# Optimization experiments

Measured on AMD Instinct MI355X. Metric: run time of the kernel, lower is better.

## Reference

```python
import jax, jax.numpy as jnp
import numpy as np
import math

B, S, H = 2, 2048, 2048
NH, HD = 16, 64  # head_dim = H // (2*NH)
LAMBDA_INIT = 0.5


def setup_inputs() -> dict:
    key = jax.random.key(0)
    ks = jax.random.split(key, 6)
    std = 1.0 / math.sqrt(H)
    hidden_states = jax.random.normal(ks[0], (B, S, H), dtype=jnp.float32)
    # Linear weights stored as [in, out] (x @ W)
    Wq = jax.random.normal(ks[1], (H, 2 * NH * HD), dtype=jnp.float32) * std
    Wk = jax.random.normal(ks[2], (H, 2 * NH * HD), dtype=jnp.float32) * std
    Wv = jax.random.normal(ks[3], (H, NH * HD), dtype=jnp.float32) * std
    Wo = jax.random.normal(ks[4], (NH * HD, H), dtype=jnp.float32) * (1.0 / math.sqrt(NH * HD))
    lambda_param = jnp.log(jnp.asarray(1.0 / math.tanh(LAMBDA_INIT), dtype=jnp.float32))
    # causal additive mask, (B, 1, S, S)
    causal = jnp.tril(jnp.ones((S, S), dtype=bool))
    attention_mask = jnp.where(causal, 0.0, jnp.finfo(jnp.float32).min)[None, None]
    attention_mask = jnp.broadcast_to(attention_mask, (B, 1, S, S))
    return {"hidden_states": hidden_states, "attention_mask": attention_mask,
            "Wq": Wq, "Wk": Wk, "Wv": Wv, "Wo": Wo, "lambda_param": lambda_param}


def reference(hidden_states, attention_mask, Wq, Wk, Wv, Wo, lambda_param):
    bsz, q_len, _ = hidden_states.shape
    scaling = HD ** -0.5

    q_all = (hidden_states @ Wq).reshape(bsz, q_len, 2 * NH, HD).transpose(0, 2, 1, 3)
    k_all = (hidden_states @ Wk).reshape(bsz, q_len, 2 * NH, HD).transpose(0, 2, 1, 3)
    v = (hidden_states @ Wv).reshape(bsz, q_len, NH, HD).transpose(0, 2, 1, 3)
    q1, q2 = q_all[:, :NH], q_all[:, NH:]
    k1, k2 = k_all[:, :NH], k_all[:, NH:]

    lam = jnp.tanh(jax.nn.softplus(lambda_param))
    scores1 = jnp.einsum('bhqd,bhkd->bhqk', q1, k1) * scaling
    scores2 = jnp.einsum('bhqd,bhkd->bhqk', q2, k2) * scaling
    attn_scores = scores1 - lam * scores2 + attention_mask
    attn_weights = jax.nn.softmax(attn_scores.astype(jnp.float32), axis=-1).astype(q1.dtype)

    attn_out = jnp.einsum('bhqk,bhkd->bhqd', attn_weights, v)
    attn_out = attn_out.transpose(0, 2, 1, 3).reshape(bsz, q_len, NH * HD)
    return attn_out @ Wo
```

## Files before the change

kernel.cpp:

```cpp
#include <hip/hip_runtime.h>
#include <hip/hip_bf16.h>

#define B_ 2
#define S_ 2048
#define H_ 2048
#define NH_ 16
#define HD_ 64
#define DQ_ 2048
#define DV_ 1024
#define QKS_ 4096

using bf16x8 = __attribute__((ext_vector_type(8))) __bf16;
using f32x4  = __attribute__((ext_vector_type(4))) float;

typedef __attribute__((address_space(1))) unsigned int u32g;
typedef __attribute__((address_space(3))) unsigned int u32l;

__device__ __forceinline__ void gload_lds16(const __bf16* g, __bf16* l) {
  __builtin_amdgcn_global_load_lds((u32g*)g, (u32l*)l, 16, 0, 0);
}

__device__ __forceinline__ int swz(int row, int colb, int strideB) {
  return row * strideB + (colb ^ (((row ^ (row >> 3)) & 7) << 4));
}
__device__ __forceinline__ int fxor(int row) { return (row ^ (row >> 3)) & 7; }


__global__ __launch_bounds__(256) void cast_hidden(const float* __restrict__ in,
                                                   __bf16* __restrict__ out, int n) {
  int i = (blockIdx.x * 256 + threadIdx.x) * 8;
  if (i >= n) return;
  float4 a = *reinterpret_cast<const float4*>(in + i);
  float4 b = *reinterpret_cast<const float4*>(in + i + 4);
  bf16x8 o;
  o[0] = (__bf16)a.x; o[1] = (__bf16)a.y; o[2] = (__bf16)a.z; o[3] = (__bf16)a.w;
  o[4] = (__bf16)b.x; o[5] = (__bf16)b.y; o[6] = (__bf16)b.z; o[7] = (__bf16)b.w;
  *reinterpret_cast<bf16x8*>(out + i) = o;
}

__global__ __launch_bounds__(256) void transpose_cast(const float* __restrict__ in,
                                                      __bf16* __restrict__ out, int R, int C) {
  __shared__ float tile[32][33];
  int tx = threadIdx.x & 31, ty = threadIdx.x >> 5;
  int c0 = blockIdx.x * 32, r0 = blockIdx.y * 32;
  for (int i = 0; i < 32; i += 8)
    tile[ty + i][tx] = in[(size_t)(r0 + ty + i) * C + c0 + tx];
  __syncthreads();
  for (int i = 0; i < 32; i += 8)
    out[(size_t)(c0 + ty + i) * R + r0 + tx] = (__bf16)tile[tx][ty + i];
}


template <typename OutT>
__global__ __launch_bounds__(256) void gemm_bt(const __bf16* __restrict__ A,
                                               const __bf16* __restrict__ Bt,
                                               OutT* __restrict__ C,
                                               int M, int N, int K) {
  __shared__ __bf16 As[2][128 * 32];
  __shared__ __bf16 Bs[2][128 * 32];
  const int nx = gridDim.x;
  int id = blockIdx.y * nx + blockIdx.x;
  const int cpx = (nx * gridDim.y) >> 3;
  id = (id & 7) * cpx + (id >> 3);
  const int bm = id / nx, bn = id % nx;

  const int tid = threadIdx.x;
  const int wid = tid >> 6, lane = tid & 63;
  const int wm = wid >> 1, wn = wid & 1;
  const int g = lane >> 4, c = lane & 15;

  f32x4 acc[4][4] = {};
  const __bf16* Abase = A + (size_t)(bm * 128) * K;
  const __bf16* Bbase = Bt + (size_t)(bn * 128) * K;
  const int srow = wid * 16 + (lane >> 2);
  const int scol = (lane & 3) * 8;
  const int nk = K >> 5;

  auto stage = [&](int p, int kt) {
    int k0 = kt * 32;
    gload_lds16(Abase + (size_t)srow * K + k0 + scol,        &As[p][(wid * 16) * 32]);
    gload_lds16(Abase + (size_t)(srow + 64) * K + k0 + scol, &As[p][(64 + wid * 16) * 32]);
    gload_lds16(Bbase + (size_t)srow * K + k0 + scol,        &Bs[p][(wid * 16) * 32]);
    gload_lds16(Bbase + (size_t)(srow + 64) * K + k0 + scol, &Bs[p][(64 + wid * 16) * 32]);
  };

  stage(0, 0);
  stage(1, 1);

  for (int kt = 0; kt < nk; ++kt) {
    const int p = kt & 1;
    if (kt + 1 < nk) {
      asm volatile("s_waitcnt vmcnt(4)" ::: "memory");
    } else {
      asm volatile("s_waitcnt vmcnt(0)" ::: "memory");
    }
    __builtin_amdgcn_s_barrier();
    __builtin_amdgcn_sched_barrier(0);

    bf16x8 af[4], bfv[4];
#pragma unroll
    for (int i = 0; i < 4; ++i)
      af[i] = *reinterpret_cast<const bf16x8*>(&As[p][(wm * 64 + i * 16 + c) * 32 + g * 8]);
#pragma unroll
    for (int i = 0; i < 4; ++i)
      bfv[i] = *reinterpret_cast<const bf16x8*>(&Bs[p][(wn * 64 + i * 16 + c) * 32 + g * 8]);
#pragma unroll
    for (int m = 0; m < 4; ++m)
#pragma unroll
      for (int n = 0; n < 4; ++n)
        acc[m][n] = __builtin_amdgcn_mfma_f32_16x16x32_bf16(af[m], bfv[n], acc[m][n], 0, 0, 0);

    __builtin_amdgcn_sched_barrier(0);
    __builtin_amdgcn_s_barrier();
    if (kt + 2 < nk) stage(p, kt + 2);
  }

#pragma unroll
  for (int m = 0; m < 4; ++m)
#pragma unroll
    for (int n = 0; n < 4; ++n)
#pragma unroll
      for (int r = 0; r < 4; ++r) {
        int row = bm * 128 + wm * 64 + m * 16 + g * 4 + r;
        int col = bn * 128 + wn * 64 + n * 16 + c;
        float v = acc[m][n][r];
        if constexpr (sizeof(OutT) == 2)
          C[(size_t)row * N + col] = (OutT)(__bf16)v;
        else
          C[(size_t)row * N + col] = v;
      }
}


template <typename OutT>
__global__ __launch_bounds__(512, 2) void gemm256(const __bf16* __restrict__ A,
                                                  const __bf16* __restrict__ Bt,
                                                  OutT* __restrict__ C,
                                                  int M, int N, int K) {
  __shared__ __bf16 As[2][256 * 64];
  __shared__ __bf16 Bs[2][256 * 64];
  const int nx = gridDim.x;
  int id = blockIdx.y * nx + blockIdx.x;
  const int cpx = (nx * gridDim.y) >> 3;
  id = (id & 7) * cpx + (id >> 3);
  const int bm = id / nx, bn = id % nx;

  const int tid = threadIdx.x;
  const int wid = tid >> 6, lane = tid & 63;
  const int wm = wid >> 2, wn = wid & 3;
  const int g = lane >> 4, c = lane & 15;

  f32x4 acc[8][4] = {};
  bf16x8 af[4][2];
  bf16x8 bfv[4][2];
  const __bf16* Abase = A + (size_t)(bm * 256) * K;
  const __bf16* Bbase = Bt + (size_t)(bn * 256) * K;
  const int niter = K >> 7;

  auto stageA = [&](int p, int half, int kt) {
#pragma unroll
    for (int j = 0; j < 2; ++j) {
      int row = half * 128 + j * 64 + wid * 8 + (lane >> 3);
      int gc = (lane & 7) ^ (row & 7);
      gload_lds16(Abase + (size_t)row * K + kt * 64 + gc * 8,
                  &As[p][(half * 128 + j * 64 + wid * 8) * 64]);
    }
  };
  auto stageB = [&](int p, int half, int kt) {
#pragma unroll
    for (int j = 0; j < 2; ++j) {
      int row = half * 128 + j * 64 + wid * 8 + (lane >> 3);
      int gc = (lane & 7) ^ (row & 7);
      gload_lds16(Bbase + (size_t)row * K + kt * 64 + gc * 8,
                  &Bs[p][(half * 128 + j * 64 + wid * 8) * 64]);
    }
  };
  auto readA = [&](int p, int m, int kk) -> bf16x8 {
    int row = wm * 128 + m * 16 + c;
    int ch = (kk * 4 + g) ^ (row & 7);
    return *reinterpret_cast<const bf16x8*>(&As[p][row * 64 + ch * 8]);
  };
  auto readB = [&](int p, int n, int kk) -> bf16x8 {
    int row = wn * 64 + n * 16 + c;
    int ch = (kk * 4 + g) ^ (row & 7);
    return *reinterpret_cast<const bf16x8*>(&Bs[p][row * 64 + ch * 8]);
  };
  auto quad = [&](int mb, int nb) {
    __builtin_amdgcn_s_setprio(1);
#pragma unroll
    for (int mi = 0; mi < 4; ++mi)
#pragma unroll
      for (int ni = 0; ni < 2; ++ni)
#pragma unroll
        for (int kk = 0; kk < 2; ++kk)
          acc[mb + mi][nb + ni] = __builtin_amdgcn_mfma_f32_16x16x32_bf16(
              af[mi][kk], bfv[nb + ni][kk], acc[mb + mi][nb + ni], 0, 0, 0);
    __builtin_amdgcn_s_setprio(0);
  };
#define BAR1_LGKM()  __builtin_amdgcn_s_barrier(); \
    asm volatile("s_waitcnt lgkmcnt(0)" ::: "memory"); \
    __builtin_amdgcn_sched_barrier(0)
#define BAR2()  __builtin_amdgcn_sched_barrier(0); __builtin_amdgcn_s_barrier()

  stageA(0, 0, 0); stageA(0, 1, 0);
  stageB(0, 0, 0); stageB(0, 1, 0);
  stageB(1, 0, 1); stageB(1, 1, 1);
  asm volatile("s_waitcnt vmcnt(0)" ::: "memory");
  __builtin_amdgcn_s_barrier();

  for (int i = 0; i < niter; ++i) {
    const int t1 = 2 * i + 1;
    const bool more = (i + 1 < niter);
#pragma unroll
    for (int mi = 0; mi < 4; ++mi) { af[mi][0] = readA(0, mi, 0); af[mi][1] = readA(0, mi, 1); }
#pragma unroll
    for (int ni = 0; ni < 2; ++ni) { bfv[ni][0] = readB(0, ni, 0); bfv[ni][1] = readB(0, ni, 1); }
    stageA(1, 0, t1);
    BAR1_LGKM(); quad(0, 0); BAR2();
#pragma unroll
    for (int ni = 2; ni < 4; ++ni) { bfv[ni][0] = readB(0, ni, 0); bfv[ni][1] = readB(0, ni, 1); }
    stageA(1, 1, t1);
    BAR1_LGKM(); quad(0, 2); BAR2();
#pragma unroll
    for (int mi = 0; mi < 4; ++mi) { af[mi][0] = readA(0, 4 + mi, 0); af[mi][1] = readA(0, 4 + mi, 1); }
    if (more) stageB(0, 0, t1 + 1);
    BAR1_LGKM(); quad(4, 0); BAR2();
    if (more) {
      stageB(0, 1, t1 + 1);
      asm volatile("s_waitcnt vmcnt(4)" ::: "memory");
    } else {
      asm volatile("s_waitcnt vmcnt(0)" ::: "memory");
    }
    __builtin_amdgcn_s_barrier();
    __builtin_amdgcn_sched_barrier(0);
    quad(4, 2); BAR2();
#pragma unroll
    for (int mi = 0; mi < 4; ++mi) { af[mi][0] = readA(1, mi, 0); af[mi][1] = readA(1, mi, 1); }
#pragma unroll
    for (int ni = 0; ni < 2; ++ni) { bfv[ni][0] = readB(1, ni, 0); bfv[ni][1] = readB(1, ni, 1); }
    if (more) stageA(0, 0, t1 + 1);
    BAR1_LGKM(); quad(0, 0); BAR2();
#pragma unroll
    for (int ni = 2; ni < 4; ++ni) { bfv[ni][0] = readB(1, ni, 0); bfv[ni][1] = readB(1, ni, 1); }
    if (more) stageA(0, 1, t1 + 1);
    BAR1_LGKM(); quad(0, 2); BAR2();
#pragma unroll
    for (int mi = 0; mi < 4; ++mi) { af[mi][0] = readA(1, 4 + mi, 0); af[mi][1] = readA(1, 4 + mi, 1); }
    if (more) stageB(1, 0, t1 + 2);
    BAR1_LGKM(); quad(4, 0); BAR2();
    if (more) {
      stageB(1, 1, t1 + 2);
      asm volatile("s_waitcnt vmcnt(4)" ::: "memory");
    } else {
      asm volatile("s_waitcnt vmcnt(0)" ::: "memory");
    }
    __builtin_amdgcn_s_barrier();
    __builtin_amdgcn_sched_barrier(0);
    quad(4, 2); BAR2();
  }
#undef BAR1_LGKM
#undef BAR2

#pragma unroll
  for (int m = 0; m < 8; ++m)
#pragma unroll
    for (int n = 0; n < 4; ++n)
#pragma unroll
      for (int r = 0; r < 4; ++r) {
        int row = bm * 256 + wm * 128 + m * 16 + g * 4 + r;
        int col = bn * 256 + wn * 64 + n * 16 + c;
        float v = acc[m][n][r];
        if constexpr (sizeof(OutT) == 2)
          C[(size_t)row * N + col] = (OutT)(__bf16)v;
        else
          C[(size_t)row * N + col] = v;
      }
}


__global__ __launch_bounds__(256, 2) void diffattn(const __bf16* __restrict__ QK,
                                                   const __bf16* __restrict__ V,
                                                   __bf16* __restrict__ OpA,
                                                   __bf16* __restrict__ OpB,
                                                   float* __restrict__ ml,
                                                   const float* __restrict__ lambda_param) {
  __shared__ __bf16 Ks[2][64 * 128];
  __shared__ __bf16 Vs[2][64 * 64];
  __shared__ __bf16 Ps[128 * 64];

  const int y = blockIdx.y;
  const int qt = ((y >> 4) & 1) ? blockIdx.x : (gridDim.x - 1 - blockIdx.x);
  const int bh = y >> 1;
  const int half = y & 1;
  const int b = bh >> 4, h = bh & 15;
  const int tid = threadIdx.x;
  const int w = tid >> 6, lane = tid & 63;
  const int g = lane >> 4, c = lane & 15;
  const float NEG_INF = -__builtin_inff();

  const float lam = tanhf(log1pf(__expf(lambda_param[0])));
  const float L2E = 1.4426950408889634f;
  const float sc1 = 0.125f * L2E;
  const float sc2 = -lam * 0.125f * L2E;

  bf16x8 qf[2][4];
#pragma unroll
  for (int fr = 0; fr < 2; ++fr) {
    int qrow = qt * 128 + w * 32 + fr * 16 + c;
    const __bf16* qbase = QK + (size_t)(b * S_ + qrow) * QKS_;
#pragma unroll
    for (int kk = 0; kk < 4; ++kk) {
      int d = kk * 32 + g * 8;
      const __bf16* src = (d < 64) ? (qbase + h * 64 + d)
                                   : (qbase + DV_ + h * 64 + (d - 64));
      float s = (d < 64) ? sc1 : sc2;
      bf16x8 raw = *reinterpret_cast<const bf16x8*>(src);
      bf16x8 ov;
#pragma unroll
      for (int i = 0; i < 8; ++i) ov[i] = (__bf16)((float)raw[i] * s);
      qf[fr][kk] = ov;
    }
  }

  f32x4 acc[2][4] = {};
  float mrow[2][4], lrow[2][4];
#pragma unroll
  for (int fr = 0; fr < 2; ++fr)
#pragma unroll
    for (int r = 0; r < 4; ++r) { mrow[fr][r] = -1e30f; lrow[fr][r] = 0.f; }

  const int kt0 = half ? (qt + 1) : 0;
  const int kt1 = half ? (2 * qt + 2) : (qt + 1);

  auto stageK = [&](int p, int kt) {
#pragma unroll
    for (int j = 0; j < 4; ++j) {
      int row = w * 16 + j * 4 + (lane >> 4);
      int gc = (lane & 15) ^ fxor(row);
      int s = kt * 64 + row;
      const __bf16* kbase = QK + (size_t)(b * S_ + s) * QKS_ + 2048;
      const __bf16* src = (gc < 8) ? (kbase + h * 64 + gc * 8)
                                   : (kbase + DV_ + h * 64 + (gc - 8) * 8);
      gload_lds16(src, &Ks[p][(w * 16 + j * 4) * 128]);
    }
  };
  auto loadV = [&](int kt, bf16x8* vv) {
#pragma unroll
    for (int j = 0; j < 2; ++j) {
      int flat = tid + j * 256;
      int kv = flat >> 3;
      int d = (flat & 7) * 8;
      vv[j] = *reinterpret_cast<const bf16x8*>(
          V + (size_t)(b * S_ + kt * 64 + kv) * DV_ + h * 64 + d);
    }
  };
  auto scatterV = [&](int p, const bf16x8* vv) {
    char* VsB = (char*)Vs[p];
#pragma unroll
    for (int j = 0; j < 2; ++j) {
      int flat = tid + j * 256;
      int kv = flat >> 3;
      int d = (flat & 7) * 8;
#pragma unroll
      for (int i = 0; i < 8; ++i)
        *reinterpret_cast<__bf16*>(VsB + swz(d + i, kv * 2, 128)) = vv[j][i];
    }
  };

  {
    stageK(0, kt0);
    bf16x8 vv[2];
    loadV(kt0, vv);
    scatterV(0, vv);
    __syncthreads();
  }

  for (int kt = kt0; kt < kt1; ++kt) {
    const int p = (kt - kt0) & 1;
    const bool pre = (kt + 1 < kt1);
    bf16x8 vv[2];
    if (pre) {
      stageK(p ^ 1, kt + 1);
      loadV(kt + 1, vv);
    }

    f32x4 sc[2][4] = {};
    char* KsB = (char*)Ks[p];
    __builtin_amdgcn_s_setprio(1);
#pragma unroll
    for (int f = 0; f < 4; ++f)
#pragma unroll
      for (int kk = 0; kk < 4; ++kk) {
        bf16x8 kf = *reinterpret_cast<const bf16x8*>(
            KsB + swz(f * 16 + c, (kk * 32 + g * 8) * 2, 256));
        sc[0][f] = __builtin_amdgcn_mfma_f32_16x16x32_bf16(qf[0][kk], kf, sc[0][f], 0, 0, 0);
        sc[1][f] = __builtin_amdgcn_mfma_f32_16x16x32_bf16(qf[1][kk], kf, sc[1][f], 0, 0, 0);
      }
    __builtin_amdgcn_s_setprio(0);

    const int dz = kt - 2 * qt;
#pragma unroll
    for (int fr = 0; fr < 2; ++fr) {
      const int wrow0 = w * 32 + fr * 16;
      float pmax[4] = {NEG_INF, NEG_INF, NEG_INF, NEG_INF};
      if (dz >= 0) {
#pragma unroll
        for (int f = 0; f < 4; ++f)
#pragma unroll
          for (int r = 0; r < 4; ++r) {
            float s = sc[fr][f][r];
            if (dz * 64 + f * 16 + c > wrow0 + g * 4 + r) s = NEG_INF;
            sc[fr][f][r] = s;
            pmax[r] = fmaxf(pmax[r], s);
          }
      } else {
#pragma unroll
        for (int f = 0; f < 4; ++f)
#pragma unroll
          for (int r = 0; r < 4; ++r)
            pmax[r] = fmaxf(pmax[r], sc[fr][f][r]);
      }

      float dm = NEG_INF;
#pragma unroll
      for (int r = 0; r < 4; ++r) dm = fmaxf(dm, pmax[r] - mrow[fr][r]);
      if (!__all(dm <= 8.0f)) {
#pragma unroll
        for (int m = 1; m < 16; m <<= 1)
#pragma unroll
          for (int r = 0; r < 4; ++r)
            pmax[r] = fmaxf(pmax[r], __shfl_xor(pmax[r], m, 64));
        float pscl[4];
#pragma unroll
        for (int r = 0; r < 4; ++r) {
          float mnew = fmaxf(mrow[fr][r], pmax[r]);
          pscl[r] = __builtin_amdgcn_exp2f(mrow[fr][r] - mnew);
          mrow[fr][r] = mnew;
        }
#pragma unroll
        for (int r = 0; r < 4; ++r) lrow[fr][r] *= pscl[r];
#pragma unroll
        for (int n = 0; n < 4; ++n)
#pragma unroll
          for (int r = 0; r < 4; ++r)
            acc[fr][n][r] *= pscl[r];
      }

      float rowsum[4] = {0.f, 0.f, 0.f, 0.f};
#pragma unroll
      for (int f = 0; f < 4; ++f)
#pragma unroll
        for (int r = 0; r < 4; ++r) {
          float pv = __builtin_amdgcn_exp2f(sc[fr][f][r] - mrow[fr][r]);
          sc[fr][f][r] = pv;
          rowsum[r] += pv;
        }
#pragma unroll
      for (int m = 1; m < 16; m <<= 1)
#pragma unroll
        for (int r = 0; r < 4; ++r)
          rowsum[r] += __shfl_xor(rowsum[r], m, 64);
#pragma unroll
      for (int r = 0; r < 4; ++r)
        lrow[fr][r] += rowsum[r];

      char* PsB = (char*)Ps;
#pragma unroll
      for (int f = 0; f < 4; ++f)
#pragma unroll
        for (int r = 0; r < 4; ++r)
          *reinterpret_cast<__bf16*>(
              PsB + swz(wrow0 + g * 4 + r, (f * 16 + c) * 2, 128)) = (__bf16)sc[fr][f][r];
    }

    {
      char* PsB = (char*)Ps;
      char* VsB = (char*)Vs[p];
      __builtin_amdgcn_s_setprio(1);
#pragma unroll
      for (int fr = 0; fr < 2; ++fr)
#pragma unroll
        for (int kc = 0; kc < 2; ++kc) {
          bf16x8 pf = *reinterpret_cast<const bf16x8*>(
              PsB + swz(w * 32 + fr * 16 + c, (kc * 32 + g * 8) * 2, 128));
#pragma unroll
          for (int n = 0; n < 4; ++n) {
            bf16x8 vf = *reinterpret_cast<const bf16x8*>(
                VsB + swz(n * 16 + c, (kc * 32 + g * 8) * 2, 128));
            acc[fr][n] = __builtin_amdgcn_mfma_f32_16x16x32_bf16(pf, vf, acc[fr][n], 0, 0, 0);
          }
        }
      __builtin_amdgcn_s_setprio(0);
    }

    if (pre) scatterV(p ^ 1, vv);
    __syncthreads();
  }

  __bf16* Op = half ? OpB : OpA;
#pragma unroll
  for (int fr = 0; fr < 2; ++fr)
#pragma unroll
    for (int n = 0; n < 4; ++n)
#pragma unroll
      for (int r = 0; r < 4; ++r) {
        int q = qt * 128 + w * 32 + fr * 16 + g * 4 + r;
        Op[(size_t)(b * S_ + q) * DV_ + h * 64 + n * 16 + c] = (__bf16)acc[fr][n][r];
      }
  if (c == 0) {
#pragma unroll
    for (int fr = 0; fr < 2; ++fr)
#pragma unroll
      for (int r = 0; r < 4; ++r) {
        int q = qt * 128 + w * 32 + fr * 16 + g * 4 + r;
        float2 v;
        v.x = mrow[fr][r];
        v.y = lrow[fr][r];
        *reinterpret_cast<float2*>(&ml[((size_t)(half * 32 + bh) * S_ + q) * 2]) = v;
      }
  }
}


__global__ __launch_bounds__(256) void merge_halves(const __bf16* __restrict__ OpA,
                                                    const __bf16* __restrict__ OpB,
                                                    const float* __restrict__ ml,
                                                    __bf16* __restrict__ AO) {
  int flat = blockIdx.x * 256 + threadIdx.x;
  int d0 = (flat & 7) * 8;
  int row = flat >> 3;
  int bh = row >> 11, q = row & 2047;
  int b = bh >> 4, h = bh & 15;
  size_t obase = (size_t)(b * S_ + q) * DV_ + h * 64 + d0;

  float2 a2 = *reinterpret_cast<const float2*>(&ml[((size_t)bh * S_ + q) * 2]);
  float2 b2 = *reinterpret_cast<const float2*>(&ml[((size_t)(32 + bh) * S_ + q) * 2]);
  float m = fmaxf(a2.x, b2.x);
  float wA = __builtin_amdgcn_exp2f(a2.x - m);
  float wB = __builtin_amdgcn_exp2f(b2.x - m);
  float inv = 1.0f / (a2.y * wA + b2.y * wB);
  wA *= inv; wB *= inv;

  bf16x8 oa = *reinterpret_cast<const bf16x8*>(OpA + obase);
  bf16x8 ob = *reinterpret_cast<const bf16x8*>(OpB + obase);
  bf16x8 o;
#pragma unroll
  for (int i = 0; i < 8; ++i)
    o[i] = (__bf16)((float)oa[i] * wA + (float)ob[i] * wB);
  *reinterpret_cast<bf16x8*>(AO + obase) = o;
}


extern "C" void kernel_launch(void* const* d_in, const int* in_sizes, int n_in,
                              void* d_out, int out_size, void* d_ws, size_t ws_size,
                              hipStream_t stream) {
  const float* hidden = (const float*)d_in[0];
  const float* Wq = (const float*)d_in[2];
  const float* Wk = (const float*)d_in[3];
  const float* Wv = (const float*)d_in[4];
  const float* Wo = (const float*)d_in[5];
  const float* lambda_param = (const float*)d_in[6];
  float* out = (float*)d_out;

  char* ws = (char*)d_ws;
  size_t off = 0;
  auto alloc = [&](size_t bytes) {
    void* p = ws + off;
    off += (bytes + 255) & ~(size_t)255;
    return p;
  };
  const int M = B_ * S_;
  __bf16* hidb = (__bf16*)alloc((size_t)M * H_ * 2);
  __bf16* TB   = (__bf16*)alloc((size_t)QKS_ * H_ * 2);
  __bf16* QKa  = (__bf16*)alloc((size_t)M * QKS_ * 2);
  __bf16* Va   = (__bf16*)((char*)TB + 4u * 1024 * 1024);
  float*  mlb  = (float*)((char*)TB + 12u * 1024 * 1024);
  __bf16* OpA  = hidb;
  __bf16* OpB  = hidb + (size_t)M * DV_;
  __bf16* AO   = hidb;
  (void)ws_size; (void)in_sizes; (void)n_in; (void)out_size;

  int nh = M * H_;
  cast_hidden<<<nh / (256 * 8), 256, 0, stream>>>(hidden, hidb, nh);

  transpose_cast<<<dim3(DQ_ / 32, H_ / 32), 256, 0, stream>>>(Wq, TB, H_, DQ_);
  transpose_cast<<<dim3(DQ_ / 32, H_ / 32), 256, 0, stream>>>(Wk, TB + (size_t)DQ_ * H_, H_, DQ_);
  gemm256<__bf16><<<dim3(QKS_ / 256, M / 256), 512, 0, stream>>>(hidb, TB, QKa, M, QKS_, H_);

  transpose_cast<<<dim3(DV_ / 32, H_ / 32), 256, 0, stream>>>(Wv, TB, H_, DV_);
  gemm_bt<__bf16><<<dim3(DV_ / 128, M / 128), 256, 0, stream>>>(hidb, TB, Va, M, DV_, H_);

  diffattn<<<dim3(S_ / 128, B_ * NH_ * 2), 256, 0, stream>>>(QKa, Va, OpA, OpB, mlb, lambda_param);
  merge_halves<<<(B_ * NH_ * S_ * HD_ / 8) / 256, 256, 0, stream>>>(OpA, OpB, mlb, AO);

  transpose_cast<<<dim3(H_ / 32, DV_ / 32), 256, 0, stream>>>(Wo, TB, DV_, H_);
  gemm_bt<float><<<dim3(H_ / 128, M / 128), 256, 0, stream>>>(AO, TB, out, M, H_, DV_);
}
```

Before: 250.9 us.

## Compute transposed S^T tiles and feed P to PV MFMA via shuffles

The QK^T MFMA operands are swapped so each lane owns a full query row's scores. Row max and sum then need only two cross-lane shuffles instead of four per row, and the softmax probabilities are packed into bf16 and redistributed with lane shuffles straight into the PV MFMA operand, removing the Ps shared-memory round trip. The output accumulators come out transposed, so the partial outputs are stored d-major and merge_halves now transposes through shared memory. This adds many shuffles per tile and a strided output layout in exchange for less LDS traffic and fewer reductions.

```diff
diff --git a/kernel.cpp b/kernel.cpp
--- a/kernel.cpp
+++ b/kernel.cpp
@@ -24,6 +24,14 @@
   return row * strideB + (colb ^ (((row ^ (row >> 3)) & 7) << 4));
 }
 __device__ __forceinline__ int fxor(int row) { return (row ^ (row >> 3)) & 7; }
+
+__device__ __forceinline__ unsigned int pk2(float a, float b) {
+  __bf16 ba = (__bf16)a, bb = (__bf16)b;
+  unsigned short ua, ub;
+  __builtin_memcpy(&ua, &ba, 2);
+  __builtin_memcpy(&ub, &bb, 2);
+  return (unsigned int)ua | ((unsigned int)ub << 16);
+}
 
 
 __global__ __launch_bounds__(256) void cast_hidden(const float* __restrict__ in,
@@ -286,7 +294,6 @@
                                                    const float* __restrict__ lambda_param) {
   __shared__ __bf16 Ks[2][64 * 128];
   __shared__ __bf16 Vs[2][64 * 64];
-  __shared__ __bf16 Ps[128 * 64];
 
   const int y = blockIdx.y;
   const int qt = ((y >> 4) & 1) ? blockIdx.x : (gridDim.x - 1 - blockIdx.x);
@@ -298,6 +305,10 @@
   const int g = lane >> 4, c = lane & 15;
   const float NEG_INF = -__builtin_inff();
 
+  const int srcA = c + 32 * (g & 1);
+  const int srcB = srcA + 16;
+  const bool hiF = ((g >> 1) & 1) != 0;
+
   const float lam = tanhf(log1pf(__expf(lambda_param[0])));
   const float L2E = 1.4426950408889634f;
   const float sc1 = 0.125f * L2E;
@@ -323,11 +334,9 @@
   }
 
   f32x4 acc[2][4] = {};
-  float mrow[2][4], lrow[2][4];
-#pragma unroll
-  for (int fr = 0; fr < 2; ++fr)
-#pragma unroll
-    for (int r = 0; r < 4; ++r) { mrow[fr][r] = -1e30f; lrow[fr][r] = 0.f; }
+  float mrow[2], lrow[2];
+#pragma unroll
+  for (int fr = 0; fr < 2; ++fr) { mrow[fr] = -1e30f; lrow[fr] = 0.f; }
 
   const int kt0 = half ? (qt + 1) : 0;
   const int kt1 = half ? (2 * qt + 2) : (qt + 1);
@@ -393,103 +402,91 @@
       for (int kk = 0; kk < 4; ++kk) {
         bf16x8 kf = *reinterpret_cast<const bf16x8*>(
             KsB + swz(f * 16 + c, (kk * 32 + g * 8) * 2, 256));
-        sc[0][f] = __builtin_amdgcn_mfma_f32_16x16x32_bf16(qf[0][kk], kf, sc[0][f], 0, 0, 0);
-        sc[1][f] = __builtin_amdgcn_mfma_f32_16x16x32_bf16(qf[1][kk], kf, sc[1][f], 0, 0, 0);
+        sc[0][f] = __builtin_amdgcn_mfma_f32_16x16x32_bf16(kf, qf[0][kk], sc[0][f], 0, 0, 0);
+        sc[1][f] = __builtin_amdgcn_mfma_f32_16x16x32_bf16(kf, qf[1][kk], sc[1][f], 0, 0, 0);
       }
     __builtin_amdgcn_s_setprio(0);
 
     const int dz = kt - 2 * qt;
+    char* VsB = (char*)Vs[p];
 #pragma unroll
     for (int fr = 0; fr < 2; ++fr) {
-      const int wrow0 = w * 32 + fr * 16;
-      float pmax[4] = {NEG_INF, NEG_INF, NEG_INF, NEG_INF};
+      const int wq = w * 32 + fr * 16 + c;
+      float pmax = NEG_INF;
       if (dz >= 0) {
 #pragma unroll
         for (int f = 0; f < 4; ++f)
 #pragma unroll
           for (int r = 0; r < 4; ++r) {
             float s = sc[fr][f][r];
-            if (dz * 64 + f * 16 + c > wrow0 + g * 4 + r) s = NEG_INF;
+            if (dz * 64 + f * 16 + g * 4 + r > wq) s = NEG_INF;
             sc[fr][f][r] = s;
-            pmax[r] = fmaxf(pmax[r], s);
+            pmax = fmaxf(pmax, s);
           }
       } else {
 #pragma unroll
         for (int f = 0; f < 4; ++f)
 #pragma unroll
           for (int r = 0; r < 4; ++r)
-            pmax[r] = fmaxf(pmax[r], sc[fr][f][r]);
-      }
-
-      float dm = NEG_INF;
-#pragma unroll
-      for (int r = 0; r < 4; ++r) dm = fmaxf(dm, pmax[r] - mrow[fr][r]);
-      if (!__all(dm <= 8.0f)) {
-#pragma unroll
-        for (int m = 1; m < 16; m <<= 1)
+            pmax = fmaxf(pmax, sc[fr][f][r]);
+      }
+
+      if (!__all(pmax - mrow[fr] <= 8.0f)) {
+        pmax = fmaxf(pmax, __shfl_xor(pmax, 16, 64));
+        pmax = fmaxf(pmax, __shfl_xor(pmax, 32, 64));
+        float mnew = fmaxf(mrow[fr], pmax);
+        float pscl = __builtin_amdgcn_exp2f(mrow[fr] - mnew);
+        mrow[fr] = mnew;
+        lrow[fr] *= pscl;
+#pragma unroll
+        for (int n = 0; n < 4; ++n)
 #pragma unroll
           for (int r = 0; r < 4; ++r)
-            pmax[r] = fmaxf(pmax[r], __shfl_xor(pmax[r], m, 64));
-        float pscl[4];
+            acc[fr][n][r] *= pscl;
+      }
+
+      float rs = 0.f;
+#pragma unroll
+      for (int f = 0; f < 4; ++f)
 #pragma unroll
         for (int r = 0; r < 4; ++r) {
-          float mnew = fmaxf(mrow[fr][r], pmax[r]);
-          pscl[r] = __builtin_amdgcn_exp2f(mrow[fr][r] - mnew);
-          mrow[fr][r] = mnew;
+          float pv = __builtin_amdgcn_exp2f(sc[fr][f][r] - mrow[fr]);
+          sc[fr][f][r] = pv;
+          rs += pv;
         }
-#pragma unroll
-        for (int r = 0; r < 4; ++r) lrow[fr][r] *= pscl[r];
-#pragma unroll
-        for (int n = 0; n < 4; ++n)
-#pragma unroll
-          for (int r = 0; r < 4; ++r)
-            acc[fr][n][r] *= pscl[r];
-      }
-
-      float rowsum[4] = {0.f, 0.f, 0.f, 0.f};
-#pragma unroll
-      for (int f = 0; f < 4; ++f)
-#pragma unroll
-        for (int r = 0; r < 4; ++r) {
-          float pv = __builtin_amdgcn_exp2f(sc[fr][f][r] - mrow[fr][r]);
-          sc[fr][f][r] = pv;
-          rowsum[r] += pv;
+      lrow[fr] += rs;
+
+      unsigned int pk[4][2];
+#pragma unroll
+      for (int f = 0; f < 4; ++f) {
+        pk[f][0] = pk2(sc[fr][f][0], sc[fr][f][1]);
+        pk[f][1] = pk2(sc[fr][f][2], sc[fr][f][3]);
+      }
+
+      __builtin_amdgcn_s_setprio(1);
+#pragma unroll
+      for (int kc = 0; kc < 2; ++kc) {
+        const int fA = kc * 2, fB = kc * 2 + 1;
+        unsigned int a0 = __shfl((int)pk[fA][0], srcA, 64);
+        unsigned int a1 = __shfl((int)pk[fA][1], srcA, 64);
+        unsigned int a2 = __shfl((int)pk[fA][0], srcB, 64);
+        unsigned int a3 = __shfl((int)pk[fA][1], srcB, 64);
+        unsigned int b0 = __shfl((int)pk[fB][0], srcA, 64);
+        unsigned int b1 = __shfl((int)pk[fB][1], srcA, 64);
+        unsigned int b2 = __shfl((int)pk[fB][0], srcB, 64);
+        unsigned int b3 = __shfl((int)pk[fB][1], srcB, 64);
+        union { unsigned int u[4]; bf16x8 v; } pu;
+        pu.u[0] = hiF ? b0 : a0;
+        pu.u[1] = hiF ? b1 : a1;
+        pu.u[2] = hiF ? b2 : a2;
+        pu.u[3] = hiF ? b3 : a3;
+#pragma unroll
+        for (int n = 0; n < 4; ++n) {
+          bf16x8 vf = *reinterpret_cast<const bf16x8*>(
+              VsB + swz(n * 16 + c, (kc * 32 + g * 8) * 2, 128));
+          acc[fr][n] = __builtin_amdgcn_mfma_f32_16x16x32_bf16(vf, pu.v, acc[fr][n], 0, 0, 0);
         }
-#pragma unroll
-      for (int m = 1; m < 16; m <<= 1)
-#pragma unroll
-        for (int r = 0; r < 4; ++r)
-          rowsum[r] += __shfl_xor(rowsum[r], m, 64);
-#pragma unroll
-      for (int r = 0; r < 4; ++r)
-        lrow[fr][r] += rowsum[r];
-
-      char* PsB = (char*)Ps;
-#pragma unroll
-      for (int f = 0; f < 4; ++f)
-#pragma unroll
-        for (int r = 0; r < 4; ++r)
-          *reinterpret_cast<__bf16*>(
-              PsB + swz(wrow0 + g * 4 + r, (f * 16 + c) * 2, 128)) = (__bf16)sc[fr][f][r];
-    }
-
-    {
-      char* PsB = (char*)Ps;
-      char* VsB = (char*)Vs[p];
-      __builtin_amdgcn_s_setprio(1);
-#pragma unroll
-      for (int fr = 0; fr < 2; ++fr)
-#pragma unroll
-        for (int kc = 0; kc < 2; ++kc) {
-          bf16x8 pf = *reinterpret_cast<const bf16x8*>(
-              PsB + swz(w * 32 + fr * 16 + c, (kc * 32 + g * 8) * 2, 128));
-#pragma unroll
-          for (int n = 0; n < 4; ++n) {
-            bf16x8 vf = *reinterpret_cast<const bf16x8*>(
-                VsB + swz(n * 16 + c, (kc * 32 + g * 8) * 2, 128));
-            acc[fr][n] = __builtin_amdgcn_mfma_f32_16x16x32_bf16(pf, vf, acc[fr][n], 0, 0, 0);
-          }
-        }
+      }
       __builtin_amdgcn_s_setprio(0);
     }
 
@@ -499,25 +496,24 @@
 
   __bf16* Op = half ? OpB : OpA;
 #pragma unroll
-  for (int fr = 0; fr < 2; ++fr)
+  for (int fr = 0; fr < 2; ++fr) {
+    int q = qt * 128 + w * 32 + fr * 16 + c;
 #pragma unroll
     for (int n = 0; n < 4; ++n)
 #pragma unroll
       for (int r = 0; r < 4; ++r) {
-        int q = qt * 128 + w * 32 + fr * 16 + g * 4 + r;
-        Op[(size_t)(b * S_ + q) * DV_ + h * 64 + n * 16 + c] = (__bf16)acc[fr][n][r];
-      }
-  if (c == 0) {
-#pragma unroll
-    for (int fr = 0; fr < 2; ++fr)
-#pragma unroll
-      for (int r = 0; r < 4; ++r) {
-        int q = qt * 128 + w * 32 + fr * 16 + g * 4 + r;
-        float2 v;
-        v.x = mrow[fr][r];
-        v.y = lrow[fr][r];
-        *reinterpret_cast<float2*>(&ml[((size_t)(half * 32 + bh) * S_ + q) * 2]) = v;
-      }
+        int d = n * 16 + g * 4 + r;
+        Op[((size_t)bh * 64 + d) * S_ + q] = (__bf16)acc[fr][n][r];
+      }
+    float lt = lrow[fr];
+    lt += __shfl_xor(lt, 16, 64);
+    lt += __shfl_xor(lt, 32, 64);
+    if (g == 0) {
+      float2 v;
+      v.x = mrow[fr];
+      v.y = lt;
+      *reinterpret_cast<float2*>(&ml[((size_t)(half * 32 + bh) * S_ + q) * 2]) = v;
+    }
   }
 }
 
@@ -526,28 +522,47 @@
                                                     const __bf16* __restrict__ OpB,
                                                     const float* __restrict__ ml,
                                                     __bf16* __restrict__ AO) {
-  int flat = blockIdx.x * 256 + threadIdx.x;
-  int d0 = (flat & 7) * 8;
-  int row = flat >> 3;
-  int bh = row >> 11, q = row & 2047;
-  int b = bh >> 4, h = bh & 15;
-  size_t obase = (size_t)(b * S_ + q) * DV_ + h * 64 + d0;
-
-  float2 a2 = *reinterpret_cast<const float2*>(&ml[((size_t)bh * S_ + q) * 2]);
-  float2 b2 = *reinterpret_cast<const float2*>(&ml[((size_t)(32 + bh) * S_ + q) * 2]);
-  float m = fmaxf(a2.x, b2.x);
-  float wA = __builtin_amdgcn_exp2f(a2.x - m);
-  float wB = __builtin_amdgcn_exp2f(b2.x - m);
-  float inv = 1.0f / (a2.y * wA + b2.y * wB);
-  wA *= inv; wB *= inv;
-
-  bf16x8 oa = *reinterpret_cast<const bf16x8*>(OpA + obase);
-  bf16x8 ob = *reinterpret_cast<const bf16x8*>(OpB + obase);
-  bf16x8 o;
-#pragma unroll
-  for (int i = 0; i < 8; ++i)
-    o[i] = (__bf16)((float)oa[i] * wA + (float)ob[i] * wB);
-  *reinterpret_cast<bf16x8*>(AO + obase) = o;
+  __shared__ __bf16 tile[64][72];
+  __shared__ float wAB[64][2];
+  const int bh = blockIdx.y;
+  const int q0 = blockIdx.x * 64;
+  const int b = bh >> 4, h = bh & 15;
+  const int t = threadIdx.x;
+
+  if (t < 64) {
+    float2 a2 = *reinterpret_cast<const float2*>(&ml[((size_t)bh * S_ + q0 + t) * 2]);
+    float2 b2 = *reinterpret_cast<const float2*>(&ml[((size_t)(32 + bh) * S_ + q0 + t) * 2]);
+    float m = fmaxf(a2.x, b2.x);
+    float wA = __builtin_amdgcn_exp2f(a2.x - m);
+    float wB = __builtin_amdgcn_exp2f(b2.x - m);
+    float inv = 1.0f / (a2.y * wA + b2.y * wB);
+    wAB[t][0] = wA * inv;
+    wAB[t][1] = wB * inv;
+  }
+  __syncthreads();
+
+#pragma unroll
+  for (int i = 0; i < 2; ++i) {
+    int d = (t >> 3) + i * 32;
+    int qc = (t & 7) * 8;
+    size_t base = ((size_t)bh * 64 + d) * S_ + q0 + qc;
+    bf16x8 oa = *reinterpret_cast<const bf16x8*>(OpA + base);
+    bf16x8 ob = *reinterpret_cast<const bf16x8*>(OpB + base);
+#pragma unroll
+    for (int j = 0; j < 8; ++j)
+      tile[d][qc + j] = (__bf16)((float)oa[j] * wAB[qc + j][0] + (float)ob[j] * wAB[qc + j][1]);
+  }
+  __syncthreads();
+
+#pragma unroll
+  for (int i = 0; i < 2; ++i) {
+    int ql = (t >> 3) + i * 32;
+    int dc = (t & 7) * 8;
+    bf16x8 o;
+#pragma unroll
+    for (int j = 0; j < 8; ++j) o[j] = tile[dc + j][ql];
+    *reinterpret_cast<bf16x8*>(AO + (size_t)(b * S_ + q0 + ql) * DV_ + h * 64 + dc) = o;
+  }
 }
 
 
@@ -574,10 +589,10 @@
   __bf16* TB   = (__bf16*)alloc((size_t)QKS_ * H_ * 2);
   __bf16* QKa  = (__bf16*)alloc((size_t)M * QKS_ * 2);
   __bf16* Va   = (__bf16*)((char*)TB + 4u * 1024 * 1024);
+  __bf16* AO   = Va;
   float*  mlb  = (float*)((char*)TB + 12u * 1024 * 1024);
   __bf16* OpA  = hidb;
   __bf16* OpB  = hidb + (size_t)M * DV_;
-  __bf16* AO   = hidb;
   (void)ws_size; (void)in_sizes; (void)n_in; (void)out_size;
 
   int nh = M * H_;
@@ -591,8 +606,9 @@
   gemm_bt<__bf16><<<dim3(DV_ / 128, M / 128), 256, 0, stream>>>(hidb, TB, Va, M, DV_, H_);
 
   diffattn<<<dim3(S_ / 128, B_ * NH_ * 2), 256, 0, stream>>>(QKa, Va, OpA, OpB, mlb, lambda_param);
-  merge_halves<<<(B_ * NH_ * S_ * HD_ / 8) / 256, 256, 0, stream>>>(OpA, OpB, mlb, AO);
 
   transpose_cast<<<dim3(H_ / 32, DV_ / 32), 256, 0, stream>>>(Wo, TB, DV_, H_);
+  merge_halves<<<dim3(S_ / 64, B_ * NH_), 256, 0, stream>>>(OpA, OpB, mlb, AO);
+
   gemm_bt<float><<<dim3(H_ / 128, M / 128), 256, 0, stream>>>(AO, TB, out, M, H_, DV_);
 }
```

Result: faster. 238.4 us (-5.0%).
